# Optimization experiments

Measured on AMD Instinct MI355X. Metric: run time of the kernel, lower is better.

Reference implementation:

```python
import jax, jax.numpy as jnp
import numpy as np
import math

B, L, D, H = 2, 2048, 2048, 16
DK = D // H  # 128

def _rope_tables(dim, max_len, base=10000.0):
    freqs = 1.0 / (base ** (np.arange(0, dim, 2, dtype=np.float32) / dim))
    t = np.arange(max_len, dtype=np.float32)
    ang = np.outer(t, freqs)  # [max_len, dim//2]
    return jnp.asarray(np.cos(ang)), jnp.asarray(np.sin(ang))

def setup_inputs() -> dict:
    key = jax.random.key(0)
    kx, kq, ko = jax.random.split(key, 3)
    x = jax.random.normal(kx, (B, L, D), dtype=jnp.float32)
    w_qkv = jax.random.normal(kq, (D, 3 * D), dtype=jnp.float32) * 0.02
    w_o = jax.random.normal(ko, (D, D), dtype=jnp.float32) * 0.02
    cos, sin = _rope_tables(DK, L)
    return {"x": x, "w_qkv": w_qkv, "w_o": w_o, "cos": cos, "sin": sin}

def _apply_rope(t, cos, sin):
    # t: [B, H, L, DK]; cos/sin: [L, DK//2]
    d2 = t.shape[-1] // 2
    t1, t2 = t[..., :d2], t[..., d2:]
    c = cos[None, None, :, :]
    s = sin[None, None, :, :]
    return jnp.concatenate([t1 * c - t2 * s, t1 * s + t2 * c], axis=-1)

def reference(x, w_qkv, w_o, cos, sin):
    b, l, d = x.shape
    qkv = (x @ w_qkv).reshape(b, l, 3, H, DK)
    q = jnp.transpose(qkv[:, :, 0], (0, 2, 1, 3))  # [B,H,L,DK]
    k = jnp.transpose(qkv[:, :, 1], (0, 2, 1, 3))
    v = jnp.transpose(qkv[:, :, 2], (0, 2, 1, 3))
    q = _apply_rope(q, cos[:l], sin[:l])
    k = _apply_rope(k, cos[:l], sin[:l])
    scores = jnp.einsum('bhqd,bhkd->bhqk', q, k) / math.sqrt(DK)
    causal = jnp.triu(jnp.ones((l, l), dtype=bool), k=1)  # total_len - L + 1 = 1
    scores = jnp.where(causal[None, None], -jnp.inf, scores)
    attn = jax.nn.softmax(scores, axis=-1)  # dropout p=0 -> identity
    out = jnp.einsum('bhqk,bhkd->bhqd', attn, v)
    out = jnp.transpose(out, (0, 2, 1, 3)).reshape(b, l, d)
    return out @ w_o, k, v
```

## Files before the change

kernel.cpp:

```cpp
#include <hip/hip_runtime.h>
#include <hip/hip_bf16.h>

#define NB 2
#define NL 2048
#define ND 2048
#define NH 16
#define NDK 128
#define SCALE2 0.12753102866606474f

#define AS1 __attribute__((address_space(1)))
#define AS3 __attribute__((address_space(3)))

typedef __attribute__((ext_vector_type(8))) __bf16 bf16x8;
typedef __attribute__((ext_vector_type(4))) float f32x4;

__device__ __forceinline__ unsigned short f2bf(float f) {
    union { float f; unsigned u; } v; v.f = f;
    return (unsigned short)((v.u + 0x7fffu + ((v.u >> 16) & 1u)) >> 16);
}
__device__ __forceinline__ float bf2f(unsigned short h) {
    union { unsigned u; float f; } v; v.u = ((unsigned)h) << 16;
    return v.f;
}

__device__ __forceinline__ void transpose_tile(const float* __restrict__ in,
                                               unsigned short* __restrict__ outp,
                                               int R, int C, int bx, int by, int tid)
{
    __shared__ float T[64][65];
    const int tr0 = by * 64;
    const int tc0 = bx * 64;
    const int r = tid >> 2;
    const int q = tid & 3;
    const float* src = in + (size_t)(tr0 + r) * C + tc0 + q * 16;
    #pragma unroll
    for (int i = 0; i < 4; i++) {
        float4 f = *(const float4*)(src + 4 * i);
        T[r][q * 16 + 4 * i + 0] = f.x;
        T[r][q * 16 + 4 * i + 1] = f.y;
        T[r][q * 16 + 4 * i + 2] = f.z;
        T[r][q * 16 + 4 * i + 3] = f.w;
    }
    __syncthreads();
    unsigned short tmp[16];
    #pragma unroll
    for (int i = 0; i < 16; i++) tmp[i] = f2bf(T[q * 16 + i][r]);
    unsigned short* dst = outp + (size_t)(tc0 + r) * R + tr0 + q * 16;
    *(uint4*)dst       = *(uint4*)&tmp[0];
    *(uint4*)(dst + 8) = *(uint4*)&tmp[8];
}

__global__ __launch_bounds__(256)
void prep_kernel(const float* __restrict__ x, unsigned short* __restrict__ x_bf,
                 const float* __restrict__ w_qkv, unsigned short* __restrict__ Wt,
                 const float* __restrict__ w_o, unsigned short* __restrict__ Wt_o)
{
    const int bid = blockIdx.x;
    const int tid = threadIdx.x;
    if (bid < 4096) {
        int i = bid * 256 + tid;
        const float4 a = ((const float4*)x)[2 * i];
        const float4 b = ((const float4*)x)[2 * i + 1];
        unsigned short t[8] = { f2bf(a.x), f2bf(a.y), f2bf(a.z), f2bf(a.w),
                                f2bf(b.x), f2bf(b.y), f2bf(b.z), f2bf(b.w) };
        ((uint4*)x_bf)[i] = *(uint4*)t;
    } else if (bid < 7168) {
        int b2 = bid - 4096;
        transpose_tile(w_qkv, Wt, ND, 3 * ND, b2 % 96, b2 / 96, tid);
    } else {
        int b3 = bid - 7168;
        transpose_tile(w_o, Wt_o, ND, ND, b3 & 31, b3 >> 5, tid);
    }
}

template<int EPI>
__global__ __launch_bounds__(256)
void gemm_bf16(const unsigned short* __restrict__ A, const unsigned short* __restrict__ Bt,
               float* __restrict__ y_dst,
               unsigned short* __restrict__ q_raw,
               float* __restrict__ k_dst, float* __restrict__ v_dst,
               int K, int NT)
{
    __shared__ __align__(16) unsigned short As[3][128][32];
    __shared__ __align__(16) unsigned short Bs[3][128][32];

    const int tid = threadIdx.x;
    const int lane = tid & 63;
    const int l16 = lane & 15, g = lane >> 4;
    const int w = tid >> 6;
    const int wr = w >> 1, wc = w & 1;

    const int cpn = NT >> 3;
    const int bid = blockIdx.x;
    const int xcd = bid & 7, local = bid >> 3;
    const int bx = xcd * cpn + local % cpn;
    const int by = local / cpn;
    const int m0 = by * 128, n0 = bx * 128;

    const int rowl = (w << 4) + (lane >> 2);
    const int swl = (rowl >> 1) & 3;
    const int kofl = ((lane & 3) ^ swl) << 3;
    const unsigned short* gA = A + (size_t)(m0 + rowl) * K + kofl;
    const unsigned short* gB = Bt + (size_t)(n0 + rowl) * K + kofl;
    const int ldsoff = (w << 10) + (lane << 4);

    f32x4 acc[4][4] = {};
    const int NTILES = K >> 5;

    auto STAGE = [&](int t, int buf) {
        const int k0 = t << 5;
        char* baseA = (char*)&As[buf][0][0] + ldsoff;
        char* baseB = (char*)&Bs[buf][0][0] + ldsoff;
        #pragma unroll
        for (int i = 0; i < 2; i++) {
            __builtin_amdgcn_global_load_lds((const AS1 void*)(gA + (size_t)i * 64 * K + k0),
                                             (AS3 void*)(baseA + i * 4096), 16, 0, 0);
            __builtin_amdgcn_global_load_lds((const AS1 void*)(gB + (size_t)i * 64 * K + k0),
                                             (AS3 void*)(baseB + i * 4096), 16, 0, 0);
        }
    };

    const int rsw = (l16 >> 1) & 3;

    STAGE(0, 0); STAGE(1, 1);

    int bufC = 0;
    for (int t = 0; t < NTILES; t++) {
        const int bufS = (bufC == 0) ? 2 : bufC - 1;
        if (t + 2 < NTILES) STAGE(t + 2, bufS);
        if (t + 2 < NTILES)      asm volatile("s_waitcnt vmcnt(8)" ::: "memory");
        else if (t + 1 < NTILES) asm volatile("s_waitcnt vmcnt(4)" ::: "memory");
        else                     asm volatile("s_waitcnt vmcnt(0)" ::: "memory");
        __builtin_amdgcn_s_barrier();
        __builtin_amdgcn_sched_barrier(0);

        const char* pa = (const char*)&As[bufC][0][0];
        const char* pb = (const char*)&Bs[bufC][0][0];
        bf16x8 af[4], bfr[4];
        #pragma unroll
        for (int r = 0; r < 4; r++) {
            int row = wr * 64 + r * 16 + l16;
            af[r] = *(const bf16x8*)(pa + row * 64 + ((g ^ rsw) << 4));
        }
        #pragma unroll
        for (int c = 0; c < 4; c++) {
            int row = wc * 64 + c * 16 + l16;
            bfr[c] = *(const bf16x8*)(pb + row * 64 + ((g ^ rsw) << 4));
        }
        #pragma unroll
        for (int r = 0; r < 4; r++)
            #pragma unroll
            for (int c = 0; c < 4; c++)
                acc[r][c] = __builtin_amdgcn_mfma_f32_16x16x32_bf16(af[r], bfr[c], acc[r][c], 0, 0, 0);

        __builtin_amdgcn_s_barrier();
        __builtin_amdgcn_sched_barrier(0);
        bufC = (bufC == 2) ? 0 : bufC + 1;
    }

    if constexpr (EPI == 0) {
        const int m3 = bx >> 4, h = bx & 15;
        #pragma unroll
        for (int r = 0; r < 4; r++) {
            int mrow = m0 + wr * 64 + r * 16 + g * 4;
            int b = mrow >> 11, l = mrow & 2047;
            size_t rb = ((size_t)(b * NH + h) * NL + l) * NDK;
            #pragma unroll
            for (int c = 0; c < 4; c++) {
                int dk = wc * 64 + c * 16 + l16;
                #pragma unroll
                for (int i = 0; i < 4; i++) {
                    float val = acc[r][c][i];
                    size_t off = rb + (size_t)i * NDK + dk;
                    if (m3 == 0) q_raw[off] = f2bf(val);
                    else if (m3 == 1) k_dst[off] = val;
                    else v_dst[off] = val;
                }
            }
        }
    } else {
        #pragma unroll
        for (int r = 0; r < 4; r++) {
            int mrow = m0 + wr * 64 + r * 16 + g * 4;
            #pragma unroll
            for (int c = 0; c < 4; c++) {
                int ncol = n0 + wc * 64 + c * 16 + l16;
                #pragma unroll
                for (int i = 0; i < 4; i++)
                    y_dst[(size_t)(mrow + i) * ND + ncol] = acc[r][c][i];
            }
        }
    }
}

__global__ __launch_bounds__(256)
void mid_kernel(float* __restrict__ kp, unsigned short* __restrict__ k_bf,
                const float* __restrict__ ct, const float* __restrict__ st,
                const float* __restrict__ v, unsigned short* __restrict__ vt)
{
    const int bid = blockIdx.x;
    const int tid = threadIdx.x;
    if (bid < 4096) {
        int idx = bid * 256 + tid;
        int d = (idx & 15) << 2;
        int rr = idx >> 4;
        size_t ro = (size_t)rr * NDK;
        int l = rr & (NL - 1);
        float4 c  = *(const float4*)(ct + l * 64 + d);
        float4 s  = *(const float4*)(st + l * 64 + d);
        float4 t1 = *(const float4*)(kp + ro + d);
        float4 t2 = *(const float4*)(kp + ro + d + 64);
        float4 o1, o2;
        o1.x = t1.x * c.x - t2.x * s.x;  o2.x = t1.x * s.x + t2.x * c.x;
        o1.y = t1.y * c.y - t2.y * s.y;  o2.y = t1.y * s.y + t2.y * c.y;
        o1.z = t1.z * c.z - t2.z * s.z;  o2.z = t1.z * s.z + t2.z * c.z;
        o1.w = t1.w * c.w - t2.w * s.w;  o2.w = t1.w * s.w + t2.w * c.w;
        *(float4*)(kp + ro + d)      = o1;
        *(float4*)(kp + ro + d + 64) = o2;
        unsigned short u1[4] = { f2bf(o1.x), f2bf(o1.y), f2bf(o1.z), f2bf(o1.w) };
        unsigned short u2[4] = { f2bf(o2.x), f2bf(o2.y), f2bf(o2.z), f2bf(o2.w) };
        *(uint2*)(k_bf + ro + d)      = *(uint2*)u1;
        *(uint2*)(k_bf + ro + d + 64) = *(uint2*)u2;
    } else {
        __shared__ float T[64][65];
        int b2 = bid - 4096;
        const int bh = b2 >> 6;
        const int l0 = ((b2 >> 1) & 31) * 64;
        const int d0 = (b2 & 1) * 64;
        const int r = tid >> 2;
        const int q = tid & 3;
        const float* src = v + (size_t)bh * NL * NDK + (size_t)(l0 + r) * NDK + d0 + q * 16;
        #pragma unroll
        for (int i = 0; i < 4; i++) {
            float4 f = *(const float4*)(src + 4 * i);
            T[r][q * 16 + 4 * i + 0] = f.x;
            T[r][q * 16 + 4 * i + 1] = f.y;
            T[r][q * 16 + 4 * i + 2] = f.z;
            T[r][q * 16 + 4 * i + 3] = f.w;
        }
        __syncthreads();
        unsigned short tmp[16];
        #pragma unroll
        for (int i = 0; i < 16; i++) tmp[i] = f2bf(T[q * 16 + i][r]);
        unsigned short* dst = vt + (size_t)bh * NDK * NL + (size_t)(d0 + r) * NL + l0 + q * 16;
        *(uint4*)dst       = *(uint4*)&tmp[0];
        *(uint4*)(dst + 8) = *(uint4*)&tmp[8];
    }
}

__global__ __launch_bounds__(256)
void attn_kernel(const unsigned short* __restrict__ q,
                 const unsigned short* __restrict__ k,
                 const unsigned short* __restrict__ vt,
                 unsigned short* __restrict__ attn_out,
                 const float* __restrict__ ct, const float* __restrict__ st)
{
    __shared__ __align__(16) unsigned short Ks[64][128];
    __shared__ __align__(16) unsigned short Vts[128][64];
    __shared__ __align__(16) unsigned short Ps[4][16][64];

    char* const ksb = (char*)&Ks[0][0];
    char* const vsb = (char*)&Vts[0][0];
    char* const psb = (char*)&Ps[0][0][0];

    const int tid = threadIdx.x, lane = tid & 63, w = tid >> 6;
    const int l16 = lane & 15, g = lane >> 4;
    const int bh = blockIdx.x;
    const int b = bh >> 4, h = bh & 15;
    const size_t base = (size_t)bh * NL * NDK;

    const int krow = tid >> 2;
    const int kq = tid & 3;
    const int kwb = krow * 256 + kq * 64;
    const int kwx = (krow & 7) << 4;
    const int vrow = tid >> 1;
    const int vh = tid & 1;
    const int vwb = vrow * 128 + vh * 64;
    const int vwx = (vrow & 7) << 4;

    const int rdx = (l16 & 7) << 4;

    const unsigned short* const kbase = k + base + (size_t)krow * NDK + kq * 32;
    const unsigned short* const vbase = vt + base + (size_t)vrow * NL + vh * 32;

    for (int half = 0; half < 2; half++) {
        const int jq = half ? (int)blockIdx.y : 31 - (int)blockIdx.y;
        const int qb = jq * 64;

        bf16x8 aq[4];
        {
            const int l = qb + w * 16 + l16;
            const unsigned short* src = q + base + (size_t)l * NDK + g * 8;
            union { bf16x8 v; unsigned short s[8]; } raw[4], outv[4];
            #pragma unroll
            for (int ks2 = 0; ks2 < 4; ks2++) raw[ks2].v = *(const bf16x8*)(src + ks2 * 32);
            const float* cb = ct + (size_t)l * 64 + g * 8;
            const float* sb = st + (size_t)l * 64 + g * 8;
            float cv[2][8], sv2[2][8];
            #pragma unroll
            for (int hh = 0; hh < 2; hh++) {
                float4 c0 = *(const float4*)(cb + 32 * hh);
                float4 c1 = *(const float4*)(cb + 32 * hh + 4);
                float4 s0 = *(const float4*)(sb + 32 * hh);
                float4 s1 = *(const float4*)(sb + 32 * hh + 4);
                cv[hh][0]=c0.x*SCALE2; cv[hh][1]=c0.y*SCALE2; cv[hh][2]=c0.z*SCALE2; cv[hh][3]=c0.w*SCALE2;
                cv[hh][4]=c1.x*SCALE2; cv[hh][5]=c1.y*SCALE2; cv[hh][6]=c1.z*SCALE2; cv[hh][7]=c1.w*SCALE2;
                sv2[hh][0]=s0.x*SCALE2; sv2[hh][1]=s0.y*SCALE2; sv2[hh][2]=s0.z*SCALE2; sv2[hh][3]=s0.w*SCALE2;
                sv2[hh][4]=s1.x*SCALE2; sv2[hh][5]=s1.y*SCALE2; sv2[hh][6]=s1.z*SCALE2; sv2[hh][7]=s1.w*SCALE2;
            }
            #pragma unroll
            for (int hh = 0; hh < 2; hh++)
                #pragma unroll
                for (int j = 0; j < 8; j++) {
                    float t1 = bf2f(raw[hh].s[j]), t2 = bf2f(raw[hh + 2].s[j]);
                    float c = cv[hh][j], s = sv2[hh][j];
                    outv[hh].s[j]     = f2bf(t1 * c - t2 * s);
                    outv[hh + 2].s[j] = f2bf(t1 * s + t2 * c);
                }
            #pragma unroll
            for (int ks2 = 0; ks2 < 4; ks2++) aq[ks2] = outv[ks2].v;
        }

        f32x4 o[8] = {};
        float m_r[4], lv[4];
        #pragma unroll
        for (int i = 0; i < 4; i++) { m_r[i] = -1e30f; lv[i] = 0.f; }

        uint4 pk0, pk1, pk2, pk3, pv0, pv1, pv2, pv3;
        {
            const unsigned short* ks = kbase;
            pk0 = *(const uint4*)(ks);
            pk1 = *(const uint4*)(ks + 8);
            pk2 = *(const uint4*)(ks + 16);
            pk3 = *(const uint4*)(ks + 24);
            const unsigned short* vs = vbase;
            pv0 = *(const uint4*)(vs);
            pv1 = *(const uint4*)(vs + 8);
            pv2 = *(const uint4*)(vs + 16);
            pv3 = *(const uint4*)(vs + 24);
        }

        for (int kv0 = 0; kv0 <= qb; kv0 += 64) {
            __syncthreads();
            *(uint4*)(ksb + ((kwb     ) ^ kwx)) = pk0;
            *(uint4*)(ksb + ((kwb + 16) ^ kwx)) = pk1;
            *(uint4*)(ksb + ((kwb + 32) ^ kwx)) = pk2;
            *(uint4*)(ksb + ((kwb + 48) ^ kwx)) = pk3;
            *(uint4*)(vsb + ((vwb     ) ^ vwx)) = pv0;
            *(uint4*)(vsb + ((vwb + 16) ^ vwx)) = pv1;
            *(uint4*)(vsb + ((vwb + 32) ^ vwx)) = pv2;
            *(uint4*)(vsb + ((vwb + 48) ^ vwx)) = pv3;
            __syncthreads();

            if (kv0 + 64 <= qb) {
                const unsigned short* ks = kbase + (size_t)(kv0 + 64) * NDK;
                pk0 = *(const uint4*)(ks);
                pk1 = *(const uint4*)(ks + 8);
                pk2 = *(const uint4*)(ks + 16);
                pk3 = *(const uint4*)(ks + 24);
                const unsigned short* vs = vbase + kv0 + 64;
                pv0 = *(const uint4*)(vs);
                pv1 = *(const uint4*)(vs + 8);
                pv2 = *(const uint4*)(vs + 16);
                pv3 = *(const uint4*)(vs + 24);
                __builtin_amdgcn_sched_barrier(0);
            }

            f32x4 sv[4];
            __builtin_amdgcn_s_setprio(1);
            #pragma unroll
            for (int cf = 0; cf < 4; cf++) {
                const int krb = (cf * 16 + l16) * 256 + g * 16;
                f32x4 a = {};
                #pragma unroll
                for (int ks2 = 0; ks2 < 4; ks2++) {
                    bf16x8 kf = *(const bf16x8*)(ksb + ((krb + 64 * ks2) ^ rdx));
                    a = __builtin_amdgcn_mfma_f32_16x16x32_bf16(aq[ks2], kf, a, 0, 0, 0);
                }
                sv[cf] = a;
            }
            __builtin_amdgcn_s_setprio(0);

            const int kvl = kv0 + l16;
            const int rowb = qb + w * 16 + g * 4;
            #pragma unroll
            for (int i = 0; i < 4; i++) {
                int row = rowb + i;
                float s0 = sv[0][i];
                float s1 = sv[1][i];
                float s2 = sv[2][i];
                float s3 = sv[3][i];
                if (kvl      > row) s0 = -1e30f;
                if (kvl + 16 > row) s1 = -1e30f;
                if (kvl + 32 > row) s2 = -1e30f;
                if (kvl + 48 > row) s3 = -1e30f;
                float mx = fmaxf(fmaxf(s0, s1), fmaxf(s2, s3));
                mx = fmaxf(mx, __shfl_xor(mx, 1));
                mx = fmaxf(mx, __shfl_xor(mx, 2));
                mx = fmaxf(mx, __shfl_xor(mx, 4));
                mx = fmaxf(mx, __shfl_xor(mx, 8));
                float mnew = fmaxf(m_r[i], mx);
                float fac = exp2f(m_r[i] - mnew);
                float p0 = exp2f(s0 - mnew);
                float p1 = exp2f(s1 - mnew);
                float p2 = exp2f(s2 - mnew);
                float p3 = exp2f(s3 - mnew);
                lv[i] = lv[i] * fac + ((p0 + p1) + (p2 + p3));
                m_r[i] = mnew;
                #pragma unroll
                for (int c8 = 0; c8 < 8; c8++) o[c8][i] *= fac;
                const int pr = g * 4 + i;
                char* pw = psb + w * 2048 + pr * 128;
                const int px = (pr & 7) << 4;
                const int cb2 = l16 << 1;
                *(unsigned short*)(pw + ((cb2)      ^ px)) = f2bf(p0);
                *(unsigned short*)(pw + ((cb2 + 32) ^ px)) = f2bf(p1);
                *(unsigned short*)(pw + ((cb2 + 64) ^ px)) = f2bf(p2);
                *(unsigned short*)(pw + ((cb2 + 96) ^ px)) = f2bf(p3);
            }
            asm volatile("s_waitcnt lgkmcnt(0)" ::: "memory");
            __builtin_amdgcn_sched_barrier(0);

            bf16x8 pf[2];
            #pragma unroll
            for (int kc = 0; kc < 2; kc++)
                pf[kc] = *(const bf16x8*)(psb + w * 2048 + l16 * 128 + ((kc * 64 + g * 16) ^ rdx));
            __builtin_amdgcn_s_setprio(1);
            #pragma unroll
            for (int c8 = 0; c8 < 8; c8++) {
                const int vrb = (c8 * 16 + l16) * 128 + g * 16;
                #pragma unroll
                for (int kc = 0; kc < 2; kc++) {
                    bf16x8 vf = *(const bf16x8*)(vsb + ((vrb + kc * 64) ^ rdx));
                    o[c8] = __builtin_amdgcn_mfma_f32_16x16x32_bf16(pf[kc], vf, o[c8], 0, 0, 0);
                }
            }
            __builtin_amdgcn_s_setprio(0);
        }

        #pragma unroll
        for (int i = 0; i < 4; i++) {
            float ls = lv[i];
            ls += __shfl_xor(ls, 1);
            ls += __shfl_xor(ls, 2);
            ls += __shfl_xor(ls, 4);
            ls += __shfl_xor(ls, 8);
            float inv = 1.0f / ls;
            int qrow = qb + w * 16 + g * 4 + i;
            size_t rb = ((size_t)(b * NL + qrow)) * ND + h * NDK;
            #pragma unroll
            for (int c8 = 0; c8 < 8; c8++)
                attn_out[rb + c8 * 16 + l16] = f2bf(o[c8][i] * inv);
        }
    }
}

__global__ void ws_signature_kernel(float* y) { if (threadIdx.x == 0) y[0] = 12345.0f; }

extern "C" void kernel_launch(void* const* d_in, const int* in_sizes, int n_in,
                              void* d_out, int out_size, void* d_ws, size_t ws_size,
                              hipStream_t stream)
{
    const float* x     = (const float*)d_in[0];
    const float* w_qkv = (const float*)d_in[1];
    const float* w_o   = (const float*)d_in[2];
    const float* ct    = (const float*)d_in[3];
    const float* st    = (const float*)d_in[4];

    const size_t NTOK = (size_t)NB * NL * ND;
    float* y_out = (float*)d_out;
    float* k_out = y_out + NTOK;
    float* v_out = y_out + 2 * NTOK;

    const size_t need = (6 * NTOK + 4 * (size_t)ND * ND) * sizeof(unsigned short);
    if (ws_size < need) {
        ws_signature_kernel<<<1, 64, 0, stream>>>(y_out);
        return;
    }
    unsigned short* x_bf  = (unsigned short*)d_ws;
    unsigned short* Wt    = x_bf + NTOK;
    unsigned short* Wt_o  = Wt + (size_t)3 * ND * ND;
    unsigned short* q_raw = Wt_o + (size_t)ND * ND;
    unsigned short* q_bf  = q_raw + NTOK;
    unsigned short* k_bf  = q_bf + NTOK;
    unsigned short* Vt    = k_bf + NTOK;
    unsigned short* a_bf  = Vt + NTOK;

    prep_kernel<<<8192, 256, 0, stream>>>(x, x_bf, w_qkv, Wt, w_o, Wt_o);
    gemm_bf16<0><<<1536, 256, 0, stream>>>(x_bf, Wt, nullptr, q_raw, k_out, v_out, ND, 48);
    mid_kernel<<<6144, 256, 0, stream>>>(k_out, k_bf, ct, st, v_out, Vt);
    attn_kernel<<<dim3(32, 16), 256, 0, stream>>>(q_raw, k_bf, Vt, a_bf, ct, st);
    gemm_bf16<1><<<512, 256, 0, stream>>>(a_bf, Wt_o, y_out, nullptr, nullptr, nullptr, ND, 16);
}
```

Measured before the change: 316.2 us.

## Process both causal query tiles in one KV sweep sharing K/V loads

The attention kernel previously handled its two paired query tiles (one far, one near the diagonal) in two sequential passes, each streaming K/V from global memory into LDS. Now both tiles' Q fragments are loaded up front and a single KV loop over the longer tile also computes the shorter tile while its range is active. This reuses each K/V LDS tile for both queries, halving global K/V traffic for the overlapping range and cutting barriers. In exchange it doubles accumulator and softmax-state registers, which can lower occupancy or cause spills.

```diff
diff --git a/kernel.cpp b/kernel.cpp
--- a/kernel.cpp
+++ b/kernel.cpp
@@ -248,6 +248,127 @@
     }
 }
 
+#define Q_LOAD(AQ, QB) {                                                                 \
+    const int l = (QB) + w * 16 + l16;                                                   \
+    const unsigned short* src = q + base + (size_t)l * NDK + g * 8;                      \
+    union { bf16x8 v; unsigned short s[8]; } raw[4], outv[4];                            \
+    _Pragma("unroll")                                                                    \
+    for (int ks2 = 0; ks2 < 4; ks2++) raw[ks2].v = *(const bf16x8*)(src + ks2 * 32);     \
+    const float* cb = ct + (size_t)l * 64 + g * 8;                                       \
+    const float* sb = st + (size_t)l * 64 + g * 8;                                       \
+    float cv[2][8], sv2[2][8];                                                           \
+    _Pragma("unroll")                                                                    \
+    for (int hh = 0; hh < 2; hh++) {                                                     \
+        float4 c0 = *(const float4*)(cb + 32 * hh);                                      \
+        float4 c1 = *(const float4*)(cb + 32 * hh + 4);                                  \
+        float4 s0 = *(const float4*)(sb + 32 * hh);                                      \
+        float4 s1 = *(const float4*)(sb + 32 * hh + 4);                                  \
+        cv[hh][0]=c0.x*SCALE2; cv[hh][1]=c0.y*SCALE2; cv[hh][2]=c0.z*SCALE2; cv[hh][3]=c0.w*SCALE2; \
+        cv[hh][4]=c1.x*SCALE2; cv[hh][5]=c1.y*SCALE2; cv[hh][6]=c1.z*SCALE2; cv[hh][7]=c1.w*SCALE2; \
+        sv2[hh][0]=s0.x*SCALE2; sv2[hh][1]=s0.y*SCALE2; sv2[hh][2]=s0.z*SCALE2; sv2[hh][3]=s0.w*SCALE2; \
+        sv2[hh][4]=s1.x*SCALE2; sv2[hh][5]=s1.y*SCALE2; sv2[hh][6]=s1.z*SCALE2; sv2[hh][7]=s1.w*SCALE2; \
+    }                                                                                    \
+    _Pragma("unroll")                                                                    \
+    for (int hh = 0; hh < 2; hh++)                                                       \
+        _Pragma("unroll")                                                                \
+        for (int j = 0; j < 8; j++) {                                                    \
+            float t1 = bf2f(raw[hh].s[j]), t2 = bf2f(raw[hh + 2].s[j]);                  \
+            float c = cv[hh][j], s = sv2[hh][j];                                         \
+            outv[hh].s[j]     = f2bf(t1 * c - t2 * s);                                   \
+            outv[hh + 2].s[j] = f2bf(t1 * s + t2 * c);                                   \
+        }                                                                                \
+    _Pragma("unroll")                                                                    \
+    for (int ks2 = 0; ks2 < 4; ks2++) AQ[ks2] = outv[ks2].v;                             \
+}
+
+#define QT_PASS(AQ, O, MR, LV, QB) {                                                     \
+    f32x4 sv[4];                                                                         \
+    __builtin_amdgcn_s_setprio(1);                                                       \
+    _Pragma("unroll")                                                                    \
+    for (int cf = 0; cf < 4; cf++) {                                                     \
+        const int krb = (cf * 16 + l16) * 256 + g * 16;                                  \
+        f32x4 a = {};                                                                    \
+        _Pragma("unroll")                                                                \
+        for (int ks2 = 0; ks2 < 4; ks2++) {                                              \
+            bf16x8 kf = *(const bf16x8*)(ksb + ((krb + 64 * ks2) ^ rdx));                \
+            a = __builtin_amdgcn_mfma_f32_16x16x32_bf16(AQ[ks2], kf, a, 0, 0, 0);        \
+        }                                                                                \
+        sv[cf] = a;                                                                      \
+    }                                                                                    \
+    __builtin_amdgcn_s_setprio(0);                                                       \
+    const int kvl = kv0 + l16;                                                           \
+    const int rowb = (QB) + w * 16 + g * 4;                                              \
+    _Pragma("unroll")                                                                    \
+    for (int i = 0; i < 4; i++) {                                                        \
+        int row = rowb + i;                                                              \
+        float s0 = sv[0][i];                                                             \
+        float s1 = sv[1][i];                                                             \
+        float s2 = sv[2][i];                                                             \
+        float s3 = sv[3][i];                                                             \
+        if (kvl      > row) s0 = -1e30f;                                                 \
+        if (kvl + 16 > row) s1 = -1e30f;                                                 \
+        if (kvl + 32 > row) s2 = -1e30f;                                                 \
+        if (kvl + 48 > row) s3 = -1e30f;                                                 \
+        float mx = fmaxf(fmaxf(s0, s1), fmaxf(s2, s3));                                  \
+        mx = fmaxf(mx, __shfl_xor(mx, 1));                                               \
+        mx = fmaxf(mx, __shfl_xor(mx, 2));                                               \
+        mx = fmaxf(mx, __shfl_xor(mx, 4));                                               \
+        mx = fmaxf(mx, __shfl_xor(mx, 8));                                               \
+        float mnew = fmaxf(MR[i], mx);                                                   \
+        float fac = exp2f(MR[i] - mnew);                                                 \
+        float p0 = exp2f(s0 - mnew);                                                     \
+        float p1 = exp2f(s1 - mnew);                                                     \
+        float p2 = exp2f(s2 - mnew);                                                     \
+        float p3 = exp2f(s3 - mnew);                                                     \
+        LV[i] = LV[i] * fac + ((p0 + p1) + (p2 + p3));                                   \
+        MR[i] = mnew;                                                                    \
+        _Pragma("unroll")                                                                \
+        for (int c8 = 0; c8 < 8; c8++) O[c8][i] *= fac;                                  \
+        const int pr = g * 4 + i;                                                        \
+        char* pw = psb + w * 2048 + pr * 128;                                            \
+        const int px = (pr & 7) << 4;                                                    \
+        const int cb2 = l16 << 1;                                                        \
+        *(unsigned short*)(pw + ((cb2)      ^ px)) = f2bf(p0);                           \
+        *(unsigned short*)(pw + ((cb2 + 32) ^ px)) = f2bf(p1);                           \
+        *(unsigned short*)(pw + ((cb2 + 64) ^ px)) = f2bf(p2);                           \
+        *(unsigned short*)(pw + ((cb2 + 96) ^ px)) = f2bf(p3);                           \
+    }                                                                                    \
+    asm volatile("s_waitcnt lgkmcnt(0)" ::: "memory");                                   \
+    __builtin_amdgcn_sched_barrier(0);                                                   \
+    bf16x8 pf[2];                                                                        \
+    _Pragma("unroll")                                                                    \
+    for (int kc = 0; kc < 2; kc++)                                                       \
+        pf[kc] = *(const bf16x8*)(psb + w * 2048 + l16 * 128 + ((kc * 64 + g * 16) ^ rdx)); \
+    __builtin_amdgcn_s_setprio(1);                                                       \
+    _Pragma("unroll")                                                                    \
+    for (int c8 = 0; c8 < 8; c8++) {                                                     \
+        const int vrb = (c8 * 16 + l16) * 128 + g * 16;                                  \
+        _Pragma("unroll")                                                                \
+        for (int kc = 0; kc < 2; kc++) {                                                 \
+            bf16x8 vf = *(const bf16x8*)(vsb + ((vrb + kc * 64) ^ rdx));                 \
+            O[c8] = __builtin_amdgcn_mfma_f32_16x16x32_bf16(pf[kc], vf, O[c8], 0, 0, 0); \
+        }                                                                                \
+    }                                                                                    \
+    __builtin_amdgcn_s_setprio(0);                                                       \
+}
+
+#define WRITE_OUT(O, LV, QB) {                                                           \
+    _Pragma("unroll")                                                                    \
+    for (int i = 0; i < 4; i++) {                                                        \
+        float ls = LV[i];                                                                \
+        ls += __shfl_xor(ls, 1);                                                         \
+        ls += __shfl_xor(ls, 2);                                                         \
+        ls += __shfl_xor(ls, 4);                                                         \
+        ls += __shfl_xor(ls, 8);                                                         \
+        float inv = 1.0f / ls;                                                           \
+        int qrow = (QB) + w * 16 + g * 4 + i;                                            \
+        size_t rb = ((size_t)(b * NL + qrow)) * ND + h * NDK;                            \
+        _Pragma("unroll")                                                                \
+        for (int c8 = 0; c8 < 8; c8++)                                                   \
+            attn_out[rb + c8 * 16 + l16] = f2bf(O[c8][i] * inv);                         \
+    }                                                                                    \
+}
+
 __global__ __launch_bounds__(256)
 void attn_kernel(const unsigned short* __restrict__ q,
                  const unsigned short* __restrict__ k,
@@ -283,176 +404,71 @@
     const unsigned short* const kbase = k + base + (size_t)krow * NDK + kq * 32;
     const unsigned short* const vbase = vt + base + (size_t)vrow * NL + vh * 32;
 
-    for (int half = 0; half < 2; half++) {
-        const int jq = half ? (int)blockIdx.y : 31 - (int)blockIdx.y;
-        const int qb = jq * 64;
-
-        bf16x8 aq[4];
-        {
-            const int l = qb + w * 16 + l16;
-            const unsigned short* src = q + base + (size_t)l * NDK + g * 8;
-            union { bf16x8 v; unsigned short s[8]; } raw[4], outv[4];
-            #pragma unroll
-            for (int ks2 = 0; ks2 < 4; ks2++) raw[ks2].v = *(const bf16x8*)(src + ks2 * 32);
-            const float* cb = ct + (size_t)l * 64 + g * 8;
-            const float* sb = st + (size_t)l * 64 + g * 8;
-            float cv[2][8], sv2[2][8];
-            #pragma unroll
-            for (int hh = 0; hh < 2; hh++) {
-                float4 c0 = *(const float4*)(cb + 32 * hh);
-                float4 c1 = *(const float4*)(cb + 32 * hh + 4);
-                float4 s0 = *(const float4*)(sb + 32 * hh);
-                float4 s1 = *(const float4*)(sb + 32 * hh + 4);
-                cv[hh][0]=c0.x*SCALE2; cv[hh][1]=c0.y*SCALE2; cv[hh][2]=c0.z*SCALE2; cv[hh][3]=c0.w*SCALE2;
-                cv[hh][4]=c1.x*SCALE2; cv[hh][5]=c1.y*SCALE2; cv[hh][6]=c1.z*SCALE2; cv[hh][7]=c1.w*SCALE2;
-                sv2[hh][0]=s0.x*SCALE2; sv2[hh][1]=s0.y*SCALE2; sv2[hh][2]=s0.z*SCALE2; sv2[hh][3]=s0.w*SCALE2;
-                sv2[hh][4]=s1.x*SCALE2; sv2[hh][5]=s1.y*SCALE2; sv2[hh][6]=s1.z*SCALE2; sv2[hh][7]=s1.w*SCALE2;
-            }
-            #pragma unroll
-            for (int hh = 0; hh < 2; hh++)
-                #pragma unroll
-                for (int j = 0; j < 8; j++) {
-                    float t1 = bf2f(raw[hh].s[j]), t2 = bf2f(raw[hh + 2].s[j]);
-                    float c = cv[hh][j], s = sv2[hh][j];
-                    outv[hh].s[j]     = f2bf(t1 * c - t2 * s);
-                    outv[hh + 2].s[j] = f2bf(t1 * s + t2 * c);
-                }
-            #pragma unroll
-            for (int ks2 = 0; ks2 < 4; ks2++) aq[ks2] = outv[ks2].v;
-        }
-
-        f32x4 o[8] = {};
-        float m_r[4], lv[4];
-        #pragma unroll
-        for (int i = 0; i < 4; i++) { m_r[i] = -1e30f; lv[i] = 0.f; }
-
-        uint4 pk0, pk1, pk2, pk3, pv0, pv1, pv2, pv3;
-        {
-            const unsigned short* ks = kbase;
+    const int jq_a = 31 - (int)blockIdx.y;
+    const int jq_b = (int)blockIdx.y;
+    const int qb_a = jq_a * 64;
+    const int qb_b = jq_b * 64;
+
+    bf16x8 aq_a[4], aq_b[4];
+    Q_LOAD(aq_a, qb_a);
+    Q_LOAD(aq_b, qb_b);
+
+    f32x4 o_a[8] = {}, o_b[8] = {};
+    float m_a[4], l_a[4], m_b[4], l_b[4];
+    #pragma unroll
+    for (int i = 0; i < 4; i++) {
+        m_a[i] = -1e30f; l_a[i] = 0.f;
+        m_b[i] = -1e30f; l_b[i] = 0.f;
+    }
+
+    uint4 pk0, pk1, pk2, pk3, pv0, pv1, pv2, pv3;
+    {
+        const unsigned short* ks = kbase;
+        pk0 = *(const uint4*)(ks);
+        pk1 = *(const uint4*)(ks + 8);
+        pk2 = *(const uint4*)(ks + 16);
+        pk3 = *(const uint4*)(ks + 24);
+        const unsigned short* vs = vbase;
+        pv0 = *(const uint4*)(vs);
+        pv1 = *(const uint4*)(vs + 8);
+        pv2 = *(const uint4*)(vs + 16);
+        pv3 = *(const uint4*)(vs + 24);
+    }
+
+    for (int kv0 = 0; kv0 <= qb_a; kv0 += 64) {
+        __syncthreads();
+        *(uint4*)(ksb + ((kwb     ) ^ kwx)) = pk0;
+        *(uint4*)(ksb + ((kwb + 16) ^ kwx)) = pk1;
+        *(uint4*)(ksb + ((kwb + 32) ^ kwx)) = pk2;
+        *(uint4*)(ksb + ((kwb + 48) ^ kwx)) = pk3;
+        *(uint4*)(vsb + ((vwb     ) ^ vwx)) = pv0;
+        *(uint4*)(vsb + ((vwb + 16) ^ vwx)) = pv1;
+        *(uint4*)(vsb + ((vwb + 32) ^ vwx)) = pv2;
+        *(uint4*)(vsb + ((vwb + 48) ^ vwx)) = pv3;
+        __syncthreads();
+
+        if (kv0 + 64 <= qb_a) {
+            const unsigned short* ks = kbase + (size_t)(kv0 + 64) * NDK;
             pk0 = *(const uint4*)(ks);
             pk1 = *(const uint4*)(ks + 8);
             pk2 = *(const uint4*)(ks + 16);
             pk3 = *(const uint4*)(ks + 24);
-            const unsigned short* vs = vbase;
+            const unsigned short* vs = vbase + kv0 + 64;
             pv0 = *(const uint4*)(vs);
             pv1 = *(const uint4*)(vs + 8);
             pv2 = *(const uint4*)(vs + 16);
             pv3 = *(const uint4*)(vs + 24);
-        }
-
-        for (int kv0 = 0; kv0 <= qb; kv0 += 64) {
-            __syncthreads();
-            *(uint4*)(ksb + ((kwb     ) ^ kwx)) = pk0;
-            *(uint4*)(ksb + ((kwb + 16) ^ kwx)) = pk1;
-            *(uint4*)(ksb + ((kwb + 32) ^ kwx)) = pk2;
-            *(uint4*)(ksb + ((kwb + 48) ^ kwx)) = pk3;
-            *(uint4*)(vsb + ((vwb     ) ^ vwx)) = pv0;
-            *(uint4*)(vsb + ((vwb + 16) ^ vwx)) = pv1;
-            *(uint4*)(vsb + ((vwb + 32) ^ vwx)) = pv2;
-            *(uint4*)(vsb + ((vwb + 48) ^ vwx)) = pv3;
-            __syncthreads();
-
-            if (kv0 + 64 <= qb) {
-                const unsigned short* ks = kbase + (size_t)(kv0 + 64) * NDK;
-                pk0 = *(const uint4*)(ks);
-                pk1 = *(const uint4*)(ks + 8);
-                pk2 = *(const uint4*)(ks + 16);
-                pk3 = *(const uint4*)(ks + 24);
-                const unsigned short* vs = vbase + kv0 + 64;
-                pv0 = *(const uint4*)(vs);
-                pv1 = *(const uint4*)(vs + 8);
-                pv2 = *(const uint4*)(vs + 16);
-                pv3 = *(const uint4*)(vs + 24);
-                __builtin_amdgcn_sched_barrier(0);
-            }
-
-            f32x4 sv[4];
-            __builtin_amdgcn_s_setprio(1);
-            #pragma unroll
-            for (int cf = 0; cf < 4; cf++) {
-                const int krb = (cf * 16 + l16) * 256 + g * 16;
-                f32x4 a = {};
-                #pragma unroll
-                for (int ks2 = 0; ks2 < 4; ks2++) {
-                    bf16x8 kf = *(const bf16x8*)(ksb + ((krb + 64 * ks2) ^ rdx));
-                    a = __builtin_amdgcn_mfma_f32_16x16x32_bf16(aq[ks2], kf, a, 0, 0, 0);
-                }
-                sv[cf] = a;
-            }
-            __builtin_amdgcn_s_setprio(0);
-
-            const int kvl = kv0 + l16;
-            const int rowb = qb + w * 16 + g * 4;
-            #pragma unroll
-            for (int i = 0; i < 4; i++) {
-                int row = rowb + i;
-                float s0 = sv[0][i];
-                float s1 = sv[1][i];
-                float s2 = sv[2][i];
-                float s3 = sv[3][i];
-                if (kvl      > row) s0 = -1e30f;
-                if (kvl + 16 > row) s1 = -1e30f;
-                if (kvl + 32 > row) s2 = -1e30f;
-                if (kvl + 48 > row) s3 = -1e30f;
-                float mx = fmaxf(fmaxf(s0, s1), fmaxf(s2, s3));
-                mx = fmaxf(mx, __shfl_xor(mx, 1));
-                mx = fmaxf(mx, __shfl_xor(mx, 2));
-                mx = fmaxf(mx, __shfl_xor(mx, 4));
-                mx = fmaxf(mx, __shfl_xor(mx, 8));
-                float mnew = fmaxf(m_r[i], mx);
-                float fac = exp2f(m_r[i] - mnew);
-                float p0 = exp2f(s0 - mnew);
-                float p1 = exp2f(s1 - mnew);
-                float p2 = exp2f(s2 - mnew);
-                float p3 = exp2f(s3 - mnew);
-                lv[i] = lv[i] * fac + ((p0 + p1) + (p2 + p3));
-                m_r[i] = mnew;
-                #pragma unroll
-                for (int c8 = 0; c8 < 8; c8++) o[c8][i] *= fac;
-                const int pr = g * 4 + i;
-                char* pw = psb + w * 2048 + pr * 128;
-                const int px = (pr & 7) << 4;
-                const int cb2 = l16 << 1;
-                *(unsigned short*)(pw + ((cb2)      ^ px)) = f2bf(p0);
-                *(unsigned short*)(pw + ((cb2 + 32) ^ px)) = f2bf(p1);
-                *(unsigned short*)(pw + ((cb2 + 64) ^ px)) = f2bf(p2);
-                *(unsigned short*)(pw + ((cb2 + 96) ^ px)) = f2bf(p3);
-            }
-            asm volatile("s_waitcnt lgkmcnt(0)" ::: "memory");
             __builtin_amdgcn_sched_barrier(0);
-
-            bf16x8 pf[2];
-            #pragma unroll
-            for (int kc = 0; kc < 2; kc++)
-                pf[kc] = *(const bf16x8*)(psb + w * 2048 + l16 * 128 + ((kc * 64 + g * 16) ^ rdx));
-            __builtin_amdgcn_s_setprio(1);
-            #pragma unroll
-            for (int c8 = 0; c8 < 8; c8++) {
-                const int vrb = (c8 * 16 + l16) * 128 + g * 16;
-                #pragma unroll
-                for (int kc = 0; kc < 2; kc++) {
-                    bf16x8 vf = *(const bf16x8*)(vsb + ((vrb + kc * 64) ^ rdx));
-                    o[c8] = __builtin_amdgcn_mfma_f32_16x16x32_bf16(pf[kc], vf, o[c8], 0, 0, 0);
-                }
-            }
-            __builtin_amdgcn_s_setprio(0);
-        }
-
-        #pragma unroll
-        for (int i = 0; i < 4; i++) {
-            float ls = lv[i];
-            ls += __shfl_xor(ls, 1);
-            ls += __shfl_xor(ls, 2);
-            ls += __shfl_xor(ls, 4);
-            ls += __shfl_xor(ls, 8);
-            float inv = 1.0f / ls;
-            int qrow = qb + w * 16 + g * 4 + i;
-            size_t rb = ((size_t)(b * NL + qrow)) * ND + h * NDK;
-            #pragma unroll
-            for (int c8 = 0; c8 < 8; c8++)
-                attn_out[rb + c8 * 16 + l16] = f2bf(o[c8][i] * inv);
-        }
-    }
+        }
+
+        QT_PASS(aq_a, o_a, m_a, l_a, qb_a);
+        if (kv0 <= qb_b) {
+            QT_PASS(aq_b, o_b, m_b, l_b, qb_b);
+        }
+    }
+
+    WRITE_OUT(o_a, l_a, qb_a);
+    WRITE_OUT(o_b, l_b, qb_b);
 }
 
 __global__ void ws_signature_kernel(float* y) { if (threadIdx.x == 0) y[0] = 12345.0f; }
```

After: 372.5 us. +17.8%, slower.
